# Kernel optimization log

Measured on AMD Instinct MI355X. Metric: run time of the kernel, lower is better.

## Reference

```python
import jax, jax.numpy as jnp
import numpy as np
from itertools import combinations, product

NQ = 10
DIM = 2 ** NQ
DEPTH = 1
ENC_PAIRS = [(q, q + 1) for q in range(0, NQ - 1, 2)] + [(q, q + 1) for q in range(1, NQ - 1, 2)]  # brick layer: even then odd
PYR = [(i, i + 1) for layer in range(NQ - 1) for i in range(NQ - layer - 1)]  # pyramid RBS wire pairs (45)
OBS_PAIRS = list(combinations(range(NQ), 2))  # 45 pairwise 2-local observables

_P = {'I': np.eye(2, dtype=np.complex128),
      'X': np.array([[0, 1], [1, 0]], dtype=np.complex128),
      'Y': np.array([[0, -1j], [1j, 0]], dtype=np.complex128),
      'Z': np.array([[1, 0], [0, -1]], dtype=np.complex128)}
_WORDS = [''.join(w) for w in product('IXYZ', repeat=2)][1:]  # PennyLane pauli_basis order, identity excluded
P15 = jnp.asarray(np.stack([np.kron(_P[w[0]], _P[w[1]]) for w in _WORDS]).astype(np.complex64))
XXm = jnp.asarray(np.kron(_P['X'], _P['X']).astype(np.complex64))
YYm = jnp.asarray(np.kron(_P['Y'], _P['Y']).astype(np.complex64))
ZZm = jnp.asarray(np.kron(_P['Z'], _P['Z']).astype(np.complex64))
I4 = jnp.eye(4, dtype=jnp.complex64)
_TRIL_I, _TRIL_J = np.tril_indices(4, -1)  # order matches create_Hermitian's count+j indexing


def _u3(t, p, l):
    c = jnp.cos(t / 2).astype(jnp.complex64)
    s = jnp.sin(t / 2).astype(jnp.complex64)
    return jnp.stack([jnp.stack([c, -jnp.exp(1j * l) * s]),
                      jnp.stack([jnp.exp(1j * p) * s, jnp.exp(1j * (p + l)) * c])])


def _ising(phi, P):
    # exp(-i*phi/2 * P) for P in {XX, YY, ZZ} (P^2 = I)
    return jnp.cos(phi / 2) * I4 - 1j * jnp.sin(phi / 2) * P


def _apply1(psi, U, w):
    # psi: (B, 2, ..., 2); single-qubit gate U (2,2) on wire w
    psi = jnp.moveaxis(psi, 1 + w, -1)
    sh = psi.shape
    out = jnp.einsum('ij,brj->bri', U, psi.reshape(sh[0], -1, 2)).reshape(sh)
    return jnp.moveaxis(out, -1, 1 + w)


def _apply2(psi, U, a, b):
    # two-qubit gate on wires (a,b), a is most-significant (PennyLane wire order). U: (4,4) or batched (B,4,4)
    psi = jnp.moveaxis(psi, (1 + a, 1 + b), (-2, -1))
    sh = psi.shape
    flat = psi.reshape(sh[0], -1, 4)
    eq = 'bij,brj->bri' if U.ndim == 3 else 'ij,brj->bri'
    out = jnp.einsum(eq, U, flat).reshape(sh)
    return jnp.moveaxis(out, (-2, -1), (1 + a, 1 + b))


def _build_H(A, B, D):
    # create_Hermitian: lower triangle A+iB, diag[0:3] = D[1:4], diag[3]=0, then h + h^dagger
    n = A.shape[0]
    h = jnp.zeros((n, 4, 4), jnp.complex64)
    h = h.at[:, _TRIL_I, _TRIL_J].set(A.astype(jnp.complex64) + 1j * B.astype(jnp.complex64))
    d = np.arange(3)
    h = h.at[:, d, d].set(D[:, 1:4].astype(jnp.complex64))
    return h + jnp.conj(jnp.swapaxes(h, -1, -2))


def setup_inputs() -> dict:
    key = jax.random.key(0)
    ks = jax.random.split(key, 9)
    f32 = jnp.float32
    return {
        'x': jax.random.normal(ks[0], (256, 512), f32),
        'W1': jax.random.normal(ks[1], (512, 256), f32) * (512 ** -0.5),
        'b1': jnp.zeros((256,), f32),
        'W2': jax.random.normal(ks[2], (256, 135), f32) * (256 ** -0.5),
        'b2': jnp.zeros((135,), f32),
        'qvit_params': 0.01 * jax.random.normal(ks[3], (DEPTH, len(PYR), 12), f32),
        'A': 2.0 * jax.random.normal(ks[4], (len(OBS_PAIRS), 6), f32),
        'B': 2.0 * jax.random.normal(ks[5], (len(OBS_PAIRS), 6), f32),
        'D': 2.0 * jax.random.normal(ks[6], (len(OBS_PAIRS), 4), f32),
    }


def reference(x, W1, b1, W2, b2, qvit_params, A, B, D):
    Bsz = x.shape[0]
    # enc_proj: Linear -> SiLU -> Linear
    enc = jax.nn.silu(x @ W1 + b1) @ W2 + b2  # (B, 135)
    # Brick-layer SpecialUnitary encoding: U = exp(i * sum theta_m P_m) via eigh
    theta = enc.reshape(Bsz, len(ENC_PAIRS), 15).astype(jnp.complex64)
    Hg = jnp.einsum('bgm,mij->bgij', theta, P15)  # Hermitian generators (B, 9, 4, 4)
    ew, V = jnp.linalg.eigh(Hg)
    Ue = jnp.einsum('bgik,bgk,bgjk->bgij', V, jnp.exp(1j * ew.astype(jnp.complex64)), jnp.conj(V))
    # |0...0>
    psi = jnp.zeros((Bsz, DIM), jnp.complex64).at[:, 0].set(1.0).reshape((Bsz,) + (2,) * NQ)
    for g, (a, b) in enumerate(ENC_PAIRS):
        psi = _apply2(psi, Ue[:, g], a, b)
    # QViT pyramid ansatz
    for ly in range(DEPTH):
        for g, (a, b) in enumerate(PYR):
            p = qvit_params[ly, g]
            psi = _apply1(psi, _u3(p[0], p[1], p[2]), a)
            psi = _apply2(psi, _ising(p[3], XXm), a, b)
            psi = _apply2(psi, _ising(p[4], YYm), a, b)
            psi = _apply2(psi, _ising(p[5], ZZm), a, b)
            psi = _apply1(psi, _u3(p[6], p[7], p[8]), a)
            psi = _apply2(psi, _ising(p[9], XXm), a, b)
            psi = _apply2(psi, _ising(p[10], YYm), a, b)
            psi = _apply2(psi, _ising(p[11], ZZm), a, b)
    # Pairwise ANO Hermitian expectations
    Hobs = _build_H(A, B, D)  # (45, 4, 4)
    outs = []
    for w, (a, b) in enumerate(OBS_PAIRS):
        pm = jnp.moveaxis(psi, (1 + a, 1 + b), (1, 2)).reshape(Bsz, 4, -1)
        outs.append(jnp.real(jnp.einsum('bir,ij,bjr->b', jnp.conj(pm), Hobs[w], pm)))
    return jnp.stack(outs, axis=1).astype(jnp.float32)
```

## Files before the change

### kernel.cpp

```cpp
#include <hip/hip_runtime.h>
#include <math.h>

#define NOBS 45
typedef float2 c32;

constexpr int W2Sc[10] = {1, 0, 7, 6, 5, 4, 3, 2, 9, 8};
constexpr int OAc[NOBS] = {
    0,0,0,0,0,0,0,0,0, 1,1,1,1,1,1,1,1, 2,2,2,2,2,2,2, 3,3,3,3,3,3,
    4,4,4,4,4, 5,5,5,5, 6,6,6, 7,7, 8};
constexpr int OBc[NOBS] = {
    1,2,3,4,5,6,7,8,9, 2,3,4,5,6,7,8,9, 3,4,5,6,7,8,9, 4,5,6,7,8,9,
    5,6,7,8,9, 6,7,8,9, 7,8,9, 8,9, 9};
constexpr int TIc[6] = {1, 2, 2, 3, 3, 3};
constexpr int TJc[6] = {0, 0, 1, 0, 1, 2};

__device__ __forceinline__ c32 cfma(c32 a, c32 b, c32 c) {
    c.x = fmaf(a.x, b.x, fmaf(-a.y, b.y, c.x));
    c.y = fmaf(a.x, b.y, fmaf(a.y, b.x, c.y));
    return c;
}
__device__ __forceinline__ c32 cmul(c32 a, c32 b) {
    return make_float2(a.x * b.x - a.y * b.y, a.x * b.y + a.y * b.x);
}

__device__ __forceinline__ float swap32f(float a) {
    auto r = __builtin_amdgcn_permlane32_swap(__float_as_uint(a), __float_as_uint(a), false, false);
    return (__uint_as_float(r[0]) + __uint_as_float(r[1])) - a;
}
__device__ __forceinline__ float pairsum32(float a) {
    auto r = __builtin_amdgcn_permlane32_swap(__float_as_uint(a), __float_as_uint(a), false, false);
    return __uint_as_float(r[0]) + __uint_as_float(r[1]);
}
__device__ __forceinline__ c32 swap32c(c32 a) {
    return make_float2(swap32f(a.x), swap32f(a.y));
}
template <int M>
__device__ __forceinline__ c32 exch(c32 a) {
    if constexpr (M == 32) return swap32c(a);
    else return make_float2(__shfl_xor(a.x, M, 64), __shfl_xor(a.y, M, 64));
}

__device__ __forceinline__ int insert2(int t, int pl, int ph) {
    int low  = t & ((1 << pl) - 1);
    int rest = t >> pl;
    int nm   = ph - 1 - pl;
    int mid  = rest & ((1 << nm) - 1);
    int high = rest >> nm;
    return low | (mid << (pl + 1)) | (high << (ph + 1));
}

template <int W>
__device__ __forceinline__ c32 pE(int r, int c) {
    if constexpr (W == 0) return make_float2((r == c) ? 1.f : 0.f, 0.f);
    else if constexpr (W == 1) return make_float2((r != c) ? 1.f : 0.f, 0.f);
    else if constexpr (W == 2) return make_float2(0.f, (r == c) ? 0.f : ((r == 0) ? -1.f : 1.f));
    else return make_float2((r == c) ? ((r == 0) ? 1.f : -1.f) : 0.f, 0.f);
}
template <int W0, int W1>
__device__ __forceinline__ void paccum(c32& H, float th, int i1, int i2, int j1, int j2) {
    c32 a = pE<W0>(i1, j1), b = pE<W1>(i2, j2);
    c32 p = cmul(a, b);
    H.x = fmaf(th, p.x, H.x);
    H.y = fmaf(th, p.y, H.y);
}

__device__ __forceinline__ void gate_LL(c32 v[4], const c32* __restrict__ U) {
    c32 n0 = cfma(U[0],  v[0], cfma(U[1],  v[1], cfma(U[2],  v[2], cmul(U[3],  v[3]))));
    c32 n1 = cfma(U[4],  v[0], cfma(U[5],  v[1], cfma(U[6],  v[2], cmul(U[7],  v[3]))));
    c32 n2 = cfma(U[8],  v[0], cfma(U[9],  v[1], cfma(U[10], v[2], cmul(U[11], v[3]))));
    c32 n3 = cfma(U[12], v[0], cfma(U[13], v[1], cfma(U[14], v[2], cmul(U[15], v[3]))));
    v[0] = n0; v[1] = n1; v[2] = n2; v[3] = n3;
}

__device__ __forceinline__ void gate_LocLane5(c32 v[4], const c32* __restrict__ U, int ln) {
    int bb = (ln >> 5) & 1;
    c32 p0 = swap32c(v[0]), p1 = swap32c(v[1]), p2 = swap32c(v[2]), p3 = swap32c(v[3]);
    int c00 = bb, c01 = 2 | bb, c10 = bb ^ 1, c11 = 2 | (bb ^ 1);
    const c32* U0 = U + bb * 4;
    const c32* U1 = U + (2 | bb) * 4;
    {
        c32 n0 = cfma(U0[c00], v[0], cfma(U0[c01], v[1], cfma(U0[c10], p0, cmul(U0[c11], p1))));
        c32 n1 = cfma(U1[c00], v[0], cfma(U1[c01], v[1], cfma(U1[c10], p0, cmul(U1[c11], p1))));
        v[0] = n0; v[1] = n1;
    }
    {
        c32 n2 = cfma(U0[c00], v[2], cfma(U0[c01], v[3], cfma(U0[c10], p2, cmul(U0[c11], p3))));
        c32 n3 = cfma(U1[c00], v[2], cfma(U1[c01], v[3], cfma(U1[c10], p2, cmul(U1[c11], p3))));
        v[2] = n2; v[3] = n3;
    }
}

template <int QA, int QB>
__device__ __forceinline__ void gate_LaneLane(c32 v[4], const c32* __restrict__ U, int ln) {
    int bA = (ln >> QA) & 1, bB = (ln >> QB) & 1;
    int r = (bA << 1) | bB;
    const c32* Ur = U + r * 4;
    c32 uS = Ur[r], uB = Ur[r ^ 1], uA = Ur[r ^ 2], uC = Ur[r ^ 3];
#pragma unroll
    for (int lc = 0; lc < 4; lc++) {
        c32 pB = exch<(1 << QB)>(v[lc]);
        c32 pA = exch<(1 << QA)>(v[lc]);
        c32 pC = exch<(1 << QA) | (1 << QB)>(v[lc]);
        v[lc] = cfma(uS, v[lc], cfma(uB, pB, cfma(uA, pA, cmul(uC, pC))));
    }
}

template <int PA, int PB>
__device__ __forceinline__ void lds_apply(const c32* __restrict__ U, c32* psi, int tid) {
    const int PL = (PA < PB) ? PA : PB, PH = (PA < PB) ? PB : PA;
    int base = insert2(tid, PL, PH);
    const int oa = 1 << PA, ob = 1 << PB;
    c32 g0 = psi[base], g1 = psi[base + ob], g2 = psi[base + oa], g3 = psi[base + oa + ob];
    c32 n0 = cfma(U[0],  g0, cfma(U[1],  g1, cfma(U[2],  g2, cmul(U[3],  g3))));
    c32 n1 = cfma(U[4],  g0, cfma(U[5],  g1, cfma(U[6],  g2, cmul(U[7],  g3))));
    c32 n2 = cfma(U[8],  g0, cfma(U[9],  g1, cfma(U[10], g2, cmul(U[11], g3))));
    c32 n3 = cfma(U[12], g0, cfma(U[13], g1, cfma(U[14], g2, cmul(U[15], g3))));
    psi[base] = n0; psi[base + ob] = n1; psi[base + oa] = n2; psi[base + oa + ob] = n3;
}
template <int PA, int PB>
__device__ __forceinline__ void gate_LDS(c32 v[4], const c32* __restrict__ U, c32* psi, int tid) {
#pragma unroll
    for (int lc = 0; lc < 4; lc++) psi[(tid << 2) | lc] = v[lc];
    __syncthreads();
    lds_apply<PA, PB>(U, psi, tid);
    __syncthreads();
#pragma unroll
    for (int lc = 0; lc < 4; lc++) v[lc] = psi[(tid << 2) | lc];
}
template <int PA1, int PB1, int PA2, int PB2>
__device__ __forceinline__ void gate_LDS2(c32 v[4], const c32* __restrict__ U1,
                                          const c32* __restrict__ U2, c32* psi, int tid) {
#pragma unroll
    for (int lc = 0; lc < 4; lc++) psi[(tid << 2) | lc] = v[lc];
    __syncthreads();
    lds_apply<PA1, PB1>(U1, psi, tid);
    __syncthreads();
    lds_apply<PA2, PB2>(U2, psi, tid);
    __syncthreads();
#pragma unroll
    for (int lc = 0; lc < 4; lc++) v[lc] = psi[(tid << 2) | lc];
}

__global__ __launch_bounds__(256, 1) void mega_kernel(
    const float* __restrict__ x,  const float* __restrict__ W1, const float* __restrict__ b1,
    const float* __restrict__ W2, const float* __restrict__ b2, const float* __restrict__ qp,
    const float* __restrict__ Am, const float* __restrict__ Bm, const float* __restrict__ Dm,
    float* __restrict__ out) {
    __shared__ c32 psiS[1024];
    __shared__ c32 UeS[144];
    __shared__ c32 GpS[720];
    __shared__ float HbS[720];
    __shared__ float encS[136];
    __shared__ float redS[180];

    const int b = blockIdx.x, t = threadIdx.x, ln = t & 63;
    float* F = (float*)psiS;

    if (t < 128) ((float4*)F)[t] = ((const float4*)(x + (size_t)b * 512))[t];
    __syncthreads();
    {
        int q = t & 63, sl = t >> 6;
        float4 a4 = make_float4(0.f, 0.f, 0.f, 0.f);
#pragma unroll 16
        for (int kk = 0; kk < 128; kk++) {
            int k = sl * 128 + kk;
            float xk = F[k];
            const float4 w = *(const float4*)(W1 + (size_t)k * 256 + q * 4);
            a4.x = fmaf(xk, w.x, a4.x); a4.y = fmaf(xk, w.y, a4.y);
            a4.z = fmaf(xk, w.z, a4.z); a4.w = fmaf(xk, w.w, a4.w);
        }
        *(float4*)(F + 512 + sl * 256 + q * 4) = a4;
    }
    __syncthreads();
    {
        float hv = b1[t] + F[512 + t] + F[768 + t] + F[1024 + t] + F[1280 + t];
        hv = hv / (1.f + __expf(-hv));
        F[1536 + t] = hv;
    }
    __syncthreads();
    if (t < 135) {
        float a2 = b2[t], a3 = 0.f;
#pragma unroll 16
        for (int k = 0; k < 128; k++) {
            a2 = fmaf(F[1536 + k],       W2[(size_t)k * 135 + t],         a2);
            a3 = fmaf(F[1536 + 128 + k], W2[(size_t)(128 + k) * 135 + t], a3);
        }
        encS[t] = a2 + a3;
    }
    __syncthreads();

    c32* Mm = psiS;
    c32* Rb = psiS + 144;
    c32* TA = psiS + 288;
    if (t < 144) {
        int m = t >> 4, e = t & 15, i = e >> 2, j = e & 3;
        int i1 = i >> 1, i2 = i & 1, j1 = j >> 1, j2 = j & 1;
        const float* th = encS + m * 15;
        c32 H = make_float2(0.f, 0.f);
        paccum<0,1>(H, th[0],  i1,i2,j1,j2); paccum<0,2>(H, th[1],  i1,i2,j1,j2);
        paccum<0,3>(H, th[2],  i1,i2,j1,j2); paccum<1,0>(H, th[3],  i1,i2,j1,j2);
        paccum<1,1>(H, th[4],  i1,i2,j1,j2); paccum<1,2>(H, th[5],  i1,i2,j1,j2);
        paccum<1,3>(H, th[6],  i1,i2,j1,j2); paccum<2,0>(H, th[7],  i1,i2,j1,j2);
        paccum<2,1>(H, th[8],  i1,i2,j1,j2); paccum<2,2>(H, th[9],  i1,i2,j1,j2);
        paccum<2,3>(H, th[10], i1,i2,j1,j2); paccum<3,0>(H, th[11], i1,i2,j1,j2);
        paccum<3,1>(H, th[12], i1,i2,j1,j2); paccum<3,2>(H, th[13], i1,i2,j1,j2);
        paccum<3,3>(H, th[14], i1,i2,j1,j2);
        const float sc = 1.f / 64.f;
        Mm[t] = make_float2(-H.y * sc, H.x * sc);
        Rb[t] = make_float2((i == j) ? 1.f : 0.f, 0.f);
    } else if (t >= 234) {
        for (int w = t - 234; w < NOBS; w += 22) {
            float* Hf = HbS + w * 16;
            Hf[0] = 2.f * Dm[w * 4 + 1];
            Hf[1] = 2.f * Dm[w * 4 + 2];
            Hf[2] = 2.f * Dm[w * 4 + 3];
            Hf[3] = 0.f;
#pragma unroll
            for (int k = 0; k < 6; k++) {
                Hf[4 + 2 * k] = 2.f * Am[w * 6 + k];
                Hf[5 + 2 * k] = 2.f * Bm[w * 6 + k];
            }
        }
    }
    __syncthreads();
    c32 Mrow[4];
    if (t < 144) {
        int m = t >> 4, i = (t & 15) >> 2;
#pragma unroll
        for (int k = 0; k < 4; k++) Mrow[k] = Mm[m * 16 + i * 4 + k];
    }
    for (int step = 0; step < 13; step++) {
        if (t < 144) {
            int m = t >> 4, e = t & 15, i = e >> 2, j = e & 3;
            const c32* cur = (step & 1) ? UeS : Rb;
            c32 acc = make_float2(0.f, 0.f);
            c32 outv;
            if (step < 7) {
#pragma unroll
                for (int k = 0; k < 4; k++) acc = cfma(Mrow[k], cur[m * 16 + k * 4 + j], acc);
                float inv = 1.f / (float)(7 - step);
                outv = make_float2(fmaf(acc.x, inv, (i == j) ? 1.f : 0.f), acc.y * inv);
            } else {
#pragma unroll
                for (int k = 0; k < 4; k++)
                    acc = cfma(cur[m * 16 + i * 4 + k], cur[m * 16 + k * 4 + j], acc);
                outv = acc;
            }
            ((step & 1) ? Rb : UeS)[t] = outv;
        } else if (t >= 144 && t < 234 && step < 8) {
            int pt = t - 144, g = pt >> 1, ih = (pt & 1) << 1;
            const float* p = qp + g * 12;
            const c32* src = ((step & 1) ? TA : GpS) + g * 16;
            c32* dst = ((step & 1) ? GpS : TA) + g * 16;
#pragma unroll
            for (int r2 = 0; r2 < 2; r2++) {
                int i = ih + r2, i1 = i >> 1, i2 = i & 1;
                c32 row[4];
                if (step == 0) {
                    float s, c; __sincosf(p[0] * 0.5f, &s, &c);
                    c32 u0, u1;
                    if (i1 == 0) { u0 = make_float2(c, 0.f);
                                   u1 = make_float2(-__cosf(p[2]) * s, -__sinf(p[2]) * s); }
                    else { u0 = make_float2(__cosf(p[1]) * s, __sinf(p[1]) * s);
                           u1 = make_float2(__cosf(p[1] + p[2]) * c, __sinf(p[1] + p[2]) * c); }
#pragma unroll
                    for (int jj = 0; jj < 4; jj++) row[jj] = make_float2(0.f, 0.f);
                    row[i2] = u0; row[2 | i2] = u1;
                } else {
                    c32 coef0, coef1; int c0, c1;
                    if (step == 1 || step == 5) {
                        float s, c; __sincosf(p[step == 1 ? 3 : 9] * 0.5f, &s, &c);
                        c0 = i; coef0 = make_float2(c, 0.f);
                        c1 = i ^ 3; coef1 = make_float2(0.f, -s);
                    } else if (step == 2 || step == 6) {
                        float s, c; __sincosf(p[step == 2 ? 4 : 10] * 0.5f, &s, &c);
                        float yy = (i == 0 || i == 3) ? 1.f : -1.f;
                        c0 = i; coef0 = make_float2(c, 0.f);
                        c1 = i ^ 3; coef1 = make_float2(0.f, s * yy);
                    } else if (step == 3 || step == 7) {
                        float s, c; __sincosf(p[step == 3 ? 5 : 11] * 0.5f, &s, &c);
                        float zz = (i == 0 || i == 3) ? 1.f : -1.f;
                        c0 = i; coef0 = make_float2(c, -s * zz);
                        c1 = i; coef1 = make_float2(0.f, 0.f);
                    } else {
                        float s, c; __sincosf(p[6] * 0.5f, &s, &c);
                        if (i1 == 0) { coef0 = make_float2(c, 0.f);
                                       coef1 = make_float2(-__cosf(p[8]) * s, -__sinf(p[8]) * s); }
                        else { coef0 = make_float2(__cosf(p[7]) * s, __sinf(p[7]) * s);
                               coef1 = make_float2(__cosf(p[7] + p[8]) * c, __sinf(p[7] + p[8]) * c); }
                        c0 = i2; c1 = 2 | i2;
                    }
#pragma unroll
                    for (int jj = 0; jj < 4; jj++)
                        row[jj] = cfma(coef0, src[c0 * 4 + jj], cmul(coef1, src[c1 * 4 + jj]));
                }
#pragma unroll
                for (int jj = 0; jj < 4; jj++) dst[i * 4 + jj] = row[jj];
            }
        }
        __syncthreads();
    }

    c32 v[4];
#pragma unroll
    for (int lc = 0; lc < 4; lc++) v[lc] = make_float2(0.f, 0.f);
    if (t == 0) v[0] = make_float2(1.f, 0.f);

    gate_LL(v, UeS + 0);
    gate_LaneLane<5, 4>(v, UeS + 16, ln);
    gate_LaneLane<3, 2>(v, UeS + 32, ln);
    gate_LaneLane<1, 0>(v, UeS + 48, ln);
    gate_LDS<9, 8>(v, UeS + 64, psiS, t);
    gate_LocLane5(v, UeS + 80, ln);
    gate_LaneLane<4, 3>(v, UeS + 96, ln);
    gate_LaneLane<2, 1>(v, UeS + 112, ln);
    gate_LDS<2, 9>(v, UeS + 128, psiS, t);

    {
        int g = 0;
        for (int layer = 0; layer < 9; layer++) {
            int amax = 8 - layer;
            gate_LL(v, GpS + (g++) * 16);
            if (amax >= 1) gate_LocLane5(v, GpS + (g++) * 16, ln);
            if (amax >= 2) gate_LaneLane<5, 4>(v, GpS + (g++) * 16, ln);
            if (amax >= 3) gate_LaneLane<4, 3>(v, GpS + (g++) * 16, ln);
            if (amax >= 4) gate_LaneLane<3, 2>(v, GpS + (g++) * 16, ln);
            if (amax >= 5) gate_LaneLane<2, 1>(v, GpS + (g++) * 16, ln);
            if (amax >= 6) gate_LaneLane<1, 0>(v, GpS + (g++) * 16, ln);
            if (amax >= 8) { gate_LDS2<2, 9, 9, 8>(v, GpS + g * 16, GpS + (g + 1) * 16, psiS, t); g += 2; }
            else if (amax >= 7) gate_LDS<2, 9>(v, GpS + (g++) * 16, psiS, t);
        }
    }

#pragma unroll
    for (int lc = 0; lc < 4; lc++) psiS[(t << 2) | lc] = v[lc];
    __syncthreads();
#pragma unroll
    for (int w0 = 0; w0 < NOBS; w0 += 5) {
        float pr[5];
#pragma unroll
        for (int u = 0; u < 5; u++) {
            const int w = w0 + u;
            const int pa = W2Sc[OAc[w]], pb = W2Sc[OBc[w]];
            const int pl = (pa < pb) ? pa : pb, phh = (pa < pb) ? pb : pa;
            int base = insert2(t, pl, phh);
            const int oa = 1 << pa, ob = 1 << pb;
            c32 vg[4];
            vg[0] = psiS[base];      vg[1] = psiS[base + ob];
            vg[2] = psiS[base + oa]; vg[3] = psiS[base + oa + ob];
            const float* Hf = HbS + w * 16;
            float r = Hf[0] * fmaf(vg[0].x, vg[0].x, vg[0].y * vg[0].y)
                    + Hf[1] * fmaf(vg[1].x, vg[1].x, vg[1].y * vg[1].y)
                    + Hf[2] * fmaf(vg[2].x, vg[2].x, vg[2].y * vg[2].y);
#pragma unroll
            for (int k = 0; k < 6; k++) {
                c32 vi = vg[TIc[k]], vj = vg[TJc[k]];
                float cx = fmaf(vi.x, vj.x, vi.y * vj.y);
                float cy = fmaf(vi.x, vj.y, -vi.y * vj.x);
                r = fmaf(Hf[4 + 2 * k], cx, r);
                r = fmaf(-Hf[5 + 2 * k], cy, r);
            }
            pr[u] = r;
        }
#pragma unroll
        for (int off = 1; off <= 16; off <<= 1) {
#pragma unroll
            for (int u = 0; u < 5; u++) pr[u] += __shfl_xor(pr[u], off, 64);
        }
#pragma unroll
        for (int u = 0; u < 5; u++) pr[u] = pairsum32(pr[u]);
        if (ln == 0) {
#pragma unroll
            for (int u = 0; u < 5; u++) redS[(w0 + u) * 4 + (t >> 6)] = pr[u];
        }
    }
    __syncthreads();
    if (t < NOBS)
        out[(size_t)b * NOBS + t] = redS[t * 4] + redS[t * 4 + 1] + redS[t * 4 + 2] + redS[t * 4 + 3];
}

extern "C" void kernel_launch(void* const* d_in, const int* in_sizes, int n_in,
                              void* d_out, int out_size, void* d_ws, size_t ws_size,
                              hipStream_t stream) {
    (void)in_sizes; (void)n_in; (void)out_size; (void)d_ws; (void)ws_size;
    const float* x  = (const float*)d_in[0];
    const float* W1 = (const float*)d_in[1];
    const float* b1 = (const float*)d_in[2];
    const float* W2 = (const float*)d_in[3];
    const float* b2 = (const float*)d_in[4];
    const float* qp = (const float*)d_in[5];
    const float* Am = (const float*)d_in[6];
    const float* Bm = (const float*)d_in[7];
    const float* Dm = (const float*)d_in[8];
    float* out = (float*)d_out;

    hipLaunchKernelGGL(mega_kernel, dim3(256), dim3(256), 0, stream,
                       x, W1, b1, W2, b2, qp, Am, Bm, Dm, out);
}
```

Before: 110.2 us.

## Remap qubits to lanes and use DPP/swizzle exchanges plus DPP reductions

```diff
diff --git a/kernel.cpp b/kernel.cpp
--- a/kernel.cpp
+++ b/kernel.cpp
@@ -4,7 +4,7 @@
 #define NOBS 45
 typedef float2 c32;
 
-constexpr int W2Sc[10] = {1, 0, 7, 6, 5, 4, 3, 2, 9, 8};
+constexpr int W2Sc[10] = {1, 0, 7, 6, 5, 3, 2, 4, 9, 8};
 constexpr int OAc[NOBS] = {
     0,0,0,0,0,0,0,0,0, 1,1,1,1,1,1,1,1, 2,2,2,2,2,2,2, 3,3,3,3,3,3,
     4,4,4,4,4, 5,5,5,5, 6,6,6, 7,7, 8};
@@ -23,21 +23,50 @@
     return make_float2(a.x * b.x - a.y * b.y, a.x * b.y + a.y * b.x);
 }
 
+template <int CTRL>
+__device__ __forceinline__ float dppf(float x) {
+    return __uint_as_float((unsigned)__builtin_amdgcn_update_dpp(
+        0, (int)__float_as_uint(x), CTRL, 0xF, 0xF, true));
+}
 __device__ __forceinline__ float swap32f(float a) {
     auto r = __builtin_amdgcn_permlane32_swap(__float_as_uint(a), __float_as_uint(a), false, false);
     return (__uint_as_float(r[0]) + __uint_as_float(r[1])) - a;
 }
-__device__ __forceinline__ float pairsum32(float a) {
-    auto r = __builtin_amdgcn_permlane32_swap(__float_as_uint(a), __float_as_uint(a), false, false);
-    return __uint_as_float(r[0]) + __uint_as_float(r[1]);
-}
-__device__ __forceinline__ c32 swap32c(c32 a) {
-    return make_float2(swap32f(a.x), swap32f(a.y));
+#if __has_builtin(__builtin_amdgcn_permlane16_swap)
+__device__ __forceinline__ float swap16f(float a) {
+    auto r = __builtin_amdgcn_permlane16_swap(__float_as_uint(a), __float_as_uint(a), false, false);
+    return (__uint_as_float(r[0]) + __uint_as_float(r[1])) - a;
+}
+#else
+__device__ __forceinline__ float swap16f(float a) { return __shfl_xor(a, 16, 64); }
+#endif
+__device__ __forceinline__ float swz4f(float a) {
+    return __uint_as_float(__builtin_amdgcn_ds_swizzle(__float_as_uint(a), 0x101F));
 }
 template <int M>
-__device__ __forceinline__ c32 exch(c32 a) {
-    if constexpr (M == 32) return swap32c(a);
-    else return make_float2(__shfl_xor(a.x, M, 64), __shfl_xor(a.y, M, 64));
+__device__ __forceinline__ float exf(float x) {
+    float r = x;
+    if constexpr ((M & 3) == 1) r = dppf<0xB1>(r);
+    else if constexpr ((M & 3) == 2) r = dppf<0x4E>(r);
+    else if constexpr ((M & 3) == 3) r = dppf<0x1B>(r);
+    if constexpr (M & 4)  r = swz4f(r);
+    if constexpr (M & 8)  r = dppf<0x128>(r);
+    if constexpr (M & 16) r = swap16f(r);
+    if constexpr (M & 32) r = swap32f(r);
+    return r;
+}
+template <int M>
+__device__ __forceinline__ c32 exch(c32 a) { return make_float2(exf<M>(a.x), exf<M>(a.y)); }
+__device__ __forceinline__ c32 swap32c(c32 a) { return make_float2(swap32f(a.x), swap32f(a.y)); }
+
+__device__ __forceinline__ float wave_reduce63(float x) {
+    x += dppf<0x111>(x);
+    x += dppf<0x112>(x);
+    x += dppf<0x114>(x);
+    x += dppf<0x118>(x);
+    x += dppf<0x142>(x);
+    x += dppf<0x143>(x);
+    return x;
 }
 
 __device__ __forceinline__ int insert2(int t, int pl, int ph) {
@@ -100,7 +129,7 @@
     for (int lc = 0; lc < 4; lc++) {
         c32 pB = exch<(1 << QB)>(v[lc]);
         c32 pA = exch<(1 << QA)>(v[lc]);
-        c32 pC = exch<(1 << QA) | (1 << QB)>(v[lc]);
+        c32 pC = exch<(1 << QA)>(pB);
         v[lc] = cfma(uS, v[lc], cfma(uB, pB, cfma(uA, pA, cmul(uC, pC))));
     }
 }
@@ -308,27 +337,28 @@
 
     gate_LL(v, UeS + 0);
     gate_LaneLane<5, 4>(v, UeS + 16, ln);
-    gate_LaneLane<3, 2>(v, UeS + 32, ln);
-    gate_LaneLane<1, 0>(v, UeS + 48, ln);
+    gate_LaneLane<3, 1>(v, UeS + 32, ln);
+    gate_LaneLane<0, 2>(v, UeS + 48, ln);
     gate_LDS<9, 8>(v, UeS + 64, psiS, t);
     gate_LocLane5(v, UeS + 80, ln);
     gate_LaneLane<4, 3>(v, UeS + 96, ln);
-    gate_LaneLane<2, 1>(v, UeS + 112, ln);
-    gate_LDS<2, 9>(v, UeS + 128, psiS, t);
+    gate_LaneLane<1, 0>(v, UeS + 112, ln);
+    gate_LDS<4, 9>(v, UeS + 128, psiS, t);
 
     {
         int g = 0;
+#pragma unroll
         for (int layer = 0; layer < 9; layer++) {
             int amax = 8 - layer;
             gate_LL(v, GpS + (g++) * 16);
             if (amax >= 1) gate_LocLane5(v, GpS + (g++) * 16, ln);
             if (amax >= 2) gate_LaneLane<5, 4>(v, GpS + (g++) * 16, ln);
             if (amax >= 3) gate_LaneLane<4, 3>(v, GpS + (g++) * 16, ln);
-            if (amax >= 4) gate_LaneLane<3, 2>(v, GpS + (g++) * 16, ln);
-            if (amax >= 5) gate_LaneLane<2, 1>(v, GpS + (g++) * 16, ln);
-            if (amax >= 6) gate_LaneLane<1, 0>(v, GpS + (g++) * 16, ln);
-            if (amax >= 8) { gate_LDS2<2, 9, 9, 8>(v, GpS + g * 16, GpS + (g + 1) * 16, psiS, t); g += 2; }
-            else if (amax >= 7) gate_LDS<2, 9>(v, GpS + (g++) * 16, psiS, t);
+            if (amax >= 4) gate_LaneLane<3, 1>(v, GpS + (g++) * 16, ln);
+            if (amax >= 5) gate_LaneLane<1, 0>(v, GpS + (g++) * 16, ln);
+            if (amax >= 6) gate_LaneLane<0, 2>(v, GpS + (g++) * 16, ln);
+            if (amax >= 8) { gate_LDS2<4, 9, 9, 8>(v, GpS + g * 16, GpS + (g + 1) * 16, psiS, t); g += 2; }
+            else if (amax >= 7) gate_LDS<4, 9>(v, GpS + (g++) * 16, psiS, t);
         }
     }
 
@@ -360,16 +390,9 @@
                 r = fmaf(Hf[4 + 2 * k], cx, r);
                 r = fmaf(-Hf[5 + 2 * k], cy, r);
             }
-            pr[u] = r;
-        }
-#pragma unroll
-        for (int off = 1; off <= 16; off <<= 1) {
-#pragma unroll
-            for (int u = 0; u < 5; u++) pr[u] += __shfl_xor(pr[u], off, 64);
-        }
-#pragma unroll
-        for (int u = 0; u < 5; u++) pr[u] = pairsum32(pr[u]);
-        if (ln == 0) {
+            pr[u] = wave_reduce63(r);
+        }
+        if (ln == 63) {
 #pragma unroll
             for (int u = 0; u < 5; u++) redS[(w0 + u) * 4 + (t >> 6)] = pr[u];
         }
```

Measured after the change: 107.6 us. -2.4%, faster.
